# Optimization experiments

Hardware: AMD Instinct MI355X
Metric: run time of the kernel (lower is better)

Reference implementation:

```python
import jax, jax.numpy as jnp
import numpy as np

B, N, M = 8, 4096, 4096
CHAMFER_W, EMD_W, UNC_W = 1.0, 0.5, 0.01


def setup_inputs() -> dict:
    key = jax.random.key(0)
    k1, k2, k3 = jax.random.split(key, 3)
    return {
        "pred_pc": jax.random.normal(k1, (B, N, 3), dtype=jnp.float32),
        "target_pc": jax.random.normal(k2, (B, M, 3), dtype=jnp.float32),
        "uncertainty": jax.random.uniform(k3, (B, N), dtype=jnp.float32),
    }


def reference(pred_pc, target_pc, uncertainty):
    # squared pairwise distances via ||p||^2 + ||t||^2 - 2 p.t  -> [B, N, M]
    pred_sq = jnp.sum(pred_pc ** 2, axis=2, keepdims=True)            # [B, N, 1]
    tgt_sq = jnp.sum(target_pc ** 2, axis=2, keepdims=True)           # [B, M, 1]
    cross = jnp.einsum('bnd,bmd->bnm', pred_pc, target_pc)            # [B, N, M]
    d2 = pred_sq + jnp.swapaxes(tgt_sq, 1, 2) - 2.0 * cross           # [B, N, M]

    # ChamferDistanceLoss: mean of min squared dists both directions
    chamfer = jnp.mean(jnp.min(d2, axis=2)) + jnp.mean(jnp.min(d2, axis=1))

    # EMDLoss: torch.cdist p=2 (euclidean), min over targets, mean
    dist = jnp.sqrt(jnp.clip(d2, 0.0))
    emd = jnp.mean(jnp.min(dist, axis=2))

    # uncertainty regularizer
    unc_reg = jnp.mean(uncertainty) * UNC_W

    total = chamfer * CHAMFER_W + emd * EMD_W + unc_reg
    return total
```

## Files before the change

kernel.cpp:

```cpp
#include <hip/hip_runtime.h>
#include <math.h>

typedef _Float16 half8 __attribute__((ext_vector_type(8)));
typedef float    f32x4 __attribute__((ext_vector_type(4)));

#define Bb 8
#define Nn 4096
#define Mm 4096
#define BLOCK 512
#define WAVES 8
#define QB 1024
#define MB 512
#define NE 8
#define NTW 8
#define MTILES (MB / 16)
#define NQ (2 * Bb * Nn)


__global__ void __launch_bounds__(BLOCK) chamfer_mfma_kernel(
    const float* __restrict__ pred,
    const float* __restrict__ targ,
    float* __restrict__ mins)
{
    __shared__ uint4 fragA[QB];
    __shared__ uint4 fragB[MB];
    __shared__ uint4 fragZ;

    const int tid  = threadIdx.x;
    const int lane = tid & 63;
    const int wave = tid >> 6;

    const int id     = blockIdx.x;
    const int eighth = id & 7;
    const int qg     = (id >> 3) & 3;
    const int b      = (id >> 5) & 7;
    const int dir    = id >> 8;

    const float* Q = dir ? targ : pred;
    const float* T = dir ? pred : targ;

    for (int s = tid; s < QB; s += BLOCK) {
        const float* g = Q + ((size_t)b * Nn + qg * QB + s) * 3;
        _Float16 xh = (_Float16)g[0], yh = (_Float16)g[1], zh = (_Float16)g[2];
        float xq = (float)xh, yq = (float)yh, zq = (float)zh;
        float pp = fmaf(xq, xq, fmaf(yq, yq, zq * zq));
        _Float16 ph = (_Float16)pp;
        _Float16 pl = (_Float16)(pp - (float)ph);
        half8 h;
        h[0] = xh; h[1] = yh; h[2] = zh; h[3] = ph;
        h[4] = (_Float16)1.0f; h[5] = pl; h[6] = (_Float16)1.0f; h[7] = (_Float16)0.0f;
        fragA[s] = *reinterpret_cast<uint4*>(&h);
    }
    {
        const float* g = T + ((size_t)b * Mm + eighth * MB + tid) * 3;
        _Float16 xh = (_Float16)g[0], yh = (_Float16)g[1], zh = (_Float16)g[2];
        float xq = (float)xh, yq = (float)yh, zq = (float)zh;
        float tt = fmaf(xq, xq, fmaf(yq, yq, zq * zq));
        _Float16 th = (_Float16)tt;
        _Float16 tl = (_Float16)(tt - (float)th);
        const _Float16 m2 = (_Float16)(-2.0f);
        half8 h;
        h[0] = m2 * xh; h[1] = m2 * yh; h[2] = m2 * zh; h[3] = (_Float16)1.0f;
        h[4] = th; h[5] = (_Float16)1.0f; h[6] = tl; h[7] = (_Float16)0.0f;
        fragB[tid] = *reinterpret_cast<uint4*>(&h);
    }
    if (tid == 0) fragZ = make_uint4(0u, 0u, 0u, 0u);
    __syncthreads();

    const bool lo16 = (lane < 16);
    const uint4* aBase = lo16 ? &fragA[wave * NTW * 16 + lane] : &fragZ;
    const int    aStep = lo16 ? 16 : 0;
    const uint4* bBase = lo16 ? &fragB[lane] : &fragZ;
    const int    bStep = lo16 ? 16 : 0;

    half8 a[NTW];
    #pragma unroll
    for (int t = 0; t < NTW; ++t)
        a[t] = *reinterpret_cast<const half8*>(aBase + t * aStep);

    f32x4 acc[NTW];
    #pragma unroll
    for (int t = 0; t < NTW; ++t) {
        acc[t][0] = __builtin_inff(); acc[t][1] = __builtin_inff();
        acc[t][2] = __builtin_inff(); acc[t][3] = __builtin_inff();
    }

    const f32x4 cz = {0.f, 0.f, 0.f, 0.f};
    for (int j = 0; j < MTILES; j += 2) {
        half8 b0 = *reinterpret_cast<const half8*>(bBase + j * bStep);
        half8 b1 = *reinterpret_cast<const half8*>(bBase + (j + 1) * bStep);
        #pragma unroll
        for (int t = 0; t < NTW; ++t) {
            f32x4 c = __builtin_amdgcn_mfma_f32_16x16x32_f16(a[t], b0, cz, 0, 0, 0);
            f32x4 d = __builtin_amdgcn_mfma_f32_16x16x32_f16(a[t], b1, cz, 0, 0, 0);
            #pragma unroll
            for (int k = 0; k < 4; ++k)
                acc[t][k] = fminf(fminf(acc[t][k], c[k]), d[k]);
        }
    }

    #pragma unroll
    for (int t = 0; t < NTW; ++t) {
        f32x4 v = acc[t];
        #pragma unroll
        for (int m = 1; m < 16; m <<= 1) {
            #pragma unroll
            for (int k = 0; k < 4; ++k)
                v[k] = fminf(v[k], __shfl_xor(v[k], m));
        }
        if ((lane & 15) == 0) {
            const int rowbase = (lane >> 4) * 4;
            const int nloc = (wave * NTW + t) * 16 + rowbase;
            const size_t qs = ((size_t)dir * Bb + b) * Nn + qg * QB + nloc;
            #pragma unroll
            for (int k = 0; k < 4; ++k)
                mins[(qs + k) * NE + eighth] = v[k];
        }
    }
}

__global__ void __launch_bounds__(256) reduce_kernel(
    const float* __restrict__ mins, const float* __restrict__ unc,
    float* __restrict__ partials)
{
    const int q = blockIdx.x * 256 + threadIdx.x;
    const float4* m4 = (const float4*)mins;

    float4 a0 = m4[2 * q],           a1 = m4[2 * q + 1];
    float4 b0 = m4[2 * (q + 32768)], b1 = m4[2 * (q + 32768) + 1];
    float vA = fminf(fminf(fminf(a0.x, a0.y), fminf(a0.z, a0.w)),
                     fminf(fminf(a1.x, a1.y), fminf(a1.z, a1.w)));
    float vB = fminf(fminf(fminf(b0.x, b0.y), fminf(b0.z, b0.w)),
                     fminf(fminf(b1.x, b1.y), fminf(b1.z, b1.w)));
    float sA = vA, sE = sqrtf(fmaxf(vA, 0.f)), sB = vB, sU = unc[q];

    #pragma unroll
    for (int off = 32; off > 0; off >>= 1) {
        sA += __shfl_down(sA, off);  sE += __shfl_down(sE, off);
        sB += __shfl_down(sB, off);  sU += __shfl_down(sU, off);
    }
    __shared__ float sw[4][4];
    const int lane = threadIdx.x & 63, wave = threadIdx.x >> 6;
    if (lane == 0) { sw[wave][0] = sA; sw[wave][1] = sE;
                     sw[wave][2] = sB; sw[wave][3] = sU; }
    __syncthreads();
    if (threadIdx.x < 4) {
        partials[blockIdx.x * 4 + threadIdx.x] =
            sw[0][threadIdx.x] + sw[1][threadIdx.x] +
            sw[2][threadIdx.x] + sw[3][threadIdx.x];
    }
}

__global__ void __launch_bounds__(64) finalize_kernel(
    const float* __restrict__ partials, float* __restrict__ out)
{
    const float4* p4 = (const float4*)partials;
    float4 s0 = p4[threadIdx.x], s1 = p4[threadIdx.x + 64];
    float sA = s0.x + s1.x, sE = s0.y + s1.y, sB = s0.z + s1.z, sU = s0.w + s1.w;
    #pragma unroll
    for (int off = 32; off > 0; off >>= 1) {
        sA += __shfl_down(sA, off);  sE += __shfl_down(sE, off);
        sB += __shfl_down(sB, off);  sU += __shfl_down(sU, off);
    }
    if (threadIdx.x == 0) {
        const float invBN = 1.0f / (float)(Bb * Nn);
        const float invBM = 1.0f / (float)(Bb * Mm);
        out[0] = (sA * invBN + sB * invBM) + 0.5f * (sE * invBN)
               + 0.01f * (sU * invBN);
    }
}

extern "C" void kernel_launch(void* const* d_in, const int* in_sizes, int n_in,
                              void* d_out, int out_size, void* d_ws, size_t ws_size,
                              hipStream_t stream) {
    const float* pred = (const float*)d_in[0];
    const float* targ = (const float*)d_in[1];
    const float* unc  = (const float*)d_in[2];
    float* out      = (float*)d_out;
    float* mins     = (float*)d_ws;
    float* partials = (float*)d_ws + (size_t)NQ * NE;

    chamfer_mfma_kernel<<<512, BLOCK, 0, stream>>>(pred, targ, mins);
    reduce_kernel<<<128, 256, 0, stream>>>(mins, unc, partials);
    finalize_kernel<<<1, 64, 0, stream>>>(partials, out);
}
```

Measured before the change: 26.49 us.

## Fuse reduction into chamfer kernel with full-M target tiles and last-block finalize

Each block now loads all 4096 target points into LDS and processes 256 queries (2 tiles per wave), so per-query minima are complete inside a block and the intermediate mins buffer is gone. The reduce and finalize kernels are replaced by an in-kernel block sum plus an atomic counter, where the last block to finish computes the final loss. This removes two kernel launches and the global round trip for partial minima. In exchange the grid drops to 256 blocks with fewer MFMA tiles per wave, which lowers the in-flight MFMA work available to hide latency. The counter also relies on the workspace starting at zero, and it wraps modulo the grid size instead of being reset.

```diff
diff --git a/kernel.cpp b/kernel.cpp
--- a/kernel.cpp
+++ b/kernel.cpp
@@ -9,50 +9,42 @@
 #define Mm 4096
 #define BLOCK 512
 #define WAVES 8
-#define QB 1024
-#define MB 512
-#define NE 8
-#define NTW 8
-#define MTILES (MB / 16)
-#define NQ (2 * Bb * Nn)
+#define QB 256
+#define NTW 2
+#define MTILES (Mm / 16)
+#define GRID 256
 
-
-__global__ void __launch_bounds__(BLOCK) chamfer_mfma_kernel(
+__global__ void __launch_bounds__(BLOCK) chamfer_fused_kernel(
     const float* __restrict__ pred,
     const float* __restrict__ targ,
-    float* __restrict__ mins)
+    const float* __restrict__ unc,
+    float4* __restrict__ psum,
+    unsigned* __restrict__ counter,
+    float* __restrict__ out)
 {
-    __shared__ uint4 fragA[QB];
-    __shared__ uint4 fragB[MB];
-    __shared__ uint4 fragZ;
+    __shared__ uint4 fragB[Mm];
+    float* wsum = (float*)fragB;
 
     const int tid  = threadIdx.x;
     const int lane = tid & 63;
     const int wave = tid >> 6;
 
-    const int id     = blockIdx.x;
-    const int eighth = id & 7;
-    const int qg     = (id >> 3) & 3;
-    const int b      = (id >> 5) & 7;
-    const int dir    = id >> 8;
+    const int id  = blockIdx.x;
+    const int qt  = id & 15;
+    const int b   = (id >> 4) & 7;
+    const int dir = id >> 7;
 
     const float* Q = dir ? targ : pred;
     const float* T = dir ? pred : targ;
 
-    for (int s = tid; s < QB; s += BLOCK) {
-        const float* g = Q + ((size_t)b * Nn + qg * QB + s) * 3;
-        _Float16 xh = (_Float16)g[0], yh = (_Float16)g[1], zh = (_Float16)g[2];
-        float xq = (float)xh, yq = (float)yh, zq = (float)zh;
-        float pp = fmaf(xq, xq, fmaf(yq, yq, zq * zq));
-        _Float16 ph = (_Float16)pp;
-        _Float16 pl = (_Float16)(pp - (float)ph);
-        half8 h;
-        h[0] = xh; h[1] = yh; h[2] = zh; h[3] = ph;
-        h[4] = (_Float16)1.0f; h[5] = pl; h[6] = (_Float16)1.0f; h[7] = (_Float16)0.0f;
-        fragA[s] = *reinterpret_cast<uint4*>(&h);
+    float su = 0.f;
+    if (tid < 32) {
+        float4 uu = ((const float4*)unc)[id * 32 + tid];
+        su = (uu.x + uu.y) + (uu.z + uu.w);
     }
-    {
-        const float* g = T + ((size_t)b * Mm + eighth * MB + tid) * 3;
+
+    for (int s = tid; s < Mm; s += BLOCK) {
+        const float* g = T + ((size_t)b * Mm + s) * 3;
         _Float16 xh = (_Float16)g[0], yh = (_Float16)g[1], zh = (_Float16)g[2];
         float xq = (float)xh, yq = (float)yh, zq = (float)zh;
         float tt = fmaf(xq, xq, fmaf(yq, yq, zq * zq));
@@ -62,111 +54,127 @@
         half8 h;
         h[0] = m2 * xh; h[1] = m2 * yh; h[2] = m2 * zh; h[3] = (_Float16)1.0f;
         h[4] = th; h[5] = (_Float16)1.0f; h[6] = tl; h[7] = (_Float16)0.0f;
-        fragB[tid] = *reinterpret_cast<uint4*>(&h);
+        fragB[s] = *reinterpret_cast<uint4*>(&h);
     }
-    if (tid == 0) fragZ = make_uint4(0u, 0u, 0u, 0u);
+
+    const bool lo16 = (lane < 16);
+    half8 a[NTW];
+    #pragma unroll
+    for (int t = 0; t < NTW; ++t) {
+        half8 h;
+        #pragma unroll
+        for (int e = 0; e < 8; ++e) h[e] = (_Float16)0.0f;
+        if (lo16) {
+            const int n = qt * QB + (wave * NTW + t) * 16 + lane;
+            const float* g = Q + ((size_t)b * Nn + n) * 3;
+            _Float16 xh = (_Float16)g[0], yh = (_Float16)g[1], zh = (_Float16)g[2];
+            float xq = (float)xh, yq = (float)yh, zq = (float)zh;
+            float pp = fmaf(xq, xq, fmaf(yq, yq, zq * zq));
+            _Float16 ph = (_Float16)pp;
+            _Float16 pl = (_Float16)(pp - (float)ph);
+            h[0] = xh; h[1] = yh; h[2] = zh; h[3] = ph;
+            h[4] = (_Float16)1.0f; h[5] = pl; h[6] = (_Float16)1.0f; h[7] = (_Float16)0.0f;
+        }
+        a[t] = h;
+    }
     __syncthreads();
 
-    const bool lo16 = (lane < 16);
-    const uint4* aBase = lo16 ? &fragA[wave * NTW * 16 + lane] : &fragZ;
-    const int    aStep = lo16 ? 16 : 0;
-    const uint4* bBase = lo16 ? &fragB[lane] : &fragZ;
-    const int    bStep = lo16 ? 16 : 0;
-
-    half8 a[NTW];
-    #pragma unroll
-    for (int t = 0; t < NTW; ++t)
-        a[t] = *reinterpret_cast<const half8*>(aBase + t * aStep);
-
-    f32x4 acc[NTW];
-    #pragma unroll
-    for (int t = 0; t < NTW; ++t) {
-        acc[t][0] = __builtin_inff(); acc[t][1] = __builtin_inff();
-        acc[t][2] = __builtin_inff(); acc[t][3] = __builtin_inff();
-    }
-
+    const int col = lane & 15;
     const f32x4 cz = {0.f, 0.f, 0.f, 0.f};
+    const float inf = __builtin_inff();
+    f32x4 acc0 = {inf, inf, inf, inf}, acc1 = acc0;
+    #pragma unroll 4
     for (int j = 0; j < MTILES; j += 2) {
-        half8 b0 = *reinterpret_cast<const half8*>(bBase + j * bStep);
-        half8 b1 = *reinterpret_cast<const half8*>(bBase + (j + 1) * bStep);
+        half8 b0 = *reinterpret_cast<const half8*>(&fragB[(j << 4) + col]);
+        half8 b1 = *reinterpret_cast<const half8*>(&fragB[((j + 1) << 4) + col]);
+        f32x4 c00 = __builtin_amdgcn_mfma_f32_16x16x32_f16(a[0], b0, cz, 0, 0, 0);
+        f32x4 c01 = __builtin_amdgcn_mfma_f32_16x16x32_f16(a[0], b1, cz, 0, 0, 0);
+        f32x4 c10 = __builtin_amdgcn_mfma_f32_16x16x32_f16(a[1], b0, cz, 0, 0, 0);
+        f32x4 c11 = __builtin_amdgcn_mfma_f32_16x16x32_f16(a[1], b1, cz, 0, 0, 0);
         #pragma unroll
-        for (int t = 0; t < NTW; ++t) {
-            f32x4 c = __builtin_amdgcn_mfma_f32_16x16x32_f16(a[t], b0, cz, 0, 0, 0);
-            f32x4 d = __builtin_amdgcn_mfma_f32_16x16x32_f16(a[t], b1, cz, 0, 0, 0);
-            #pragma unroll
-            for (int k = 0; k < 4; ++k)
-                acc[t][k] = fminf(fminf(acc[t][k], c[k]), d[k]);
+        for (int k = 0; k < 4; ++k) {
+            acc0[k] = fminf(fminf(acc0[k], c00[k]), c01[k]);
+            acc1[k] = fminf(fminf(acc1[k], c10[k]), c11[k]);
         }
     }
 
+    float s1 = 0.f, s2 = 0.f;
     #pragma unroll
     for (int t = 0; t < NTW; ++t) {
-        f32x4 v = acc[t];
+        f32x4 v = t ? acc1 : acc0;
         #pragma unroll
         for (int m = 1; m < 16; m <<= 1) {
             #pragma unroll
             for (int k = 0; k < 4; ++k)
                 v[k] = fminf(v[k], __shfl_xor(v[k], m));
         }
-        if ((lane & 15) == 0) {
-            const int rowbase = (lane >> 4) * 4;
-            const int nloc = (wave * NTW + t) * 16 + rowbase;
-            const size_t qs = ((size_t)dir * Bb + b) * Nn + qg * QB + nloc;
+        if (col == 0) {
             #pragma unroll
-            for (int k = 0; k < 4; ++k)
-                mins[(qs + k) * NE + eighth] = v[k];
+            for (int k = 0; k < 4; ++k) {
+                const float d2 = v[k];
+                s1 += d2;
+                s2 += sqrtf(fmaxf(d2, 0.f));
+            }
         }
     }
-}
+    #pragma unroll
+    for (int m = 1; m < 64; m <<= 1) {
+        s1 += __shfl_xor(s1, m);
+        s2 += __shfl_xor(s2, m);
+        su += __shfl_xor(su, m);
+    }
 
-__global__ void __launch_bounds__(256) reduce_kernel(
-    const float* __restrict__ mins, const float* __restrict__ unc,
-    float* __restrict__ partials)
-{
-    const int q = blockIdx.x * 256 + threadIdx.x;
-    const float4* m4 = (const float4*)mins;
-
-    float4 a0 = m4[2 * q],           a1 = m4[2 * q + 1];
-    float4 b0 = m4[2 * (q + 32768)], b1 = m4[2 * (q + 32768) + 1];
-    float vA = fminf(fminf(fminf(a0.x, a0.y), fminf(a0.z, a0.w)),
-                     fminf(fminf(a1.x, a1.y), fminf(a1.z, a1.w)));
-    float vB = fminf(fminf(fminf(b0.x, b0.y), fminf(b0.z, b0.w)),
-                     fminf(fminf(b1.x, b1.y), fminf(b1.z, b1.w)));
-    float sA = vA, sE = sqrtf(fmaxf(vA, 0.f)), sB = vB, sU = unc[q];
-
-    #pragma unroll
-    for (int off = 32; off > 0; off >>= 1) {
-        sA += __shfl_down(sA, off);  sE += __shfl_down(sE, off);
-        sB += __shfl_down(sB, off);  sU += __shfl_down(sU, off);
+    __syncthreads();
+    if (lane == 0) {
+        wsum[wave * 4 + 0] = s1;
+        wsum[wave * 4 + 1] = s2;
+        wsum[wave * 4 + 2] = su;
     }
-    __shared__ float sw[4][4];
-    const int lane = threadIdx.x & 63, wave = threadIdx.x >> 6;
-    if (lane == 0) { sw[wave][0] = sA; sw[wave][1] = sE;
-                     sw[wave][2] = sB; sw[wave][3] = sU; }
     __syncthreads();
-    if (threadIdx.x < 4) {
-        partials[blockIdx.x * 4 + threadIdx.x] =
-            sw[0][threadIdx.x] + sw[1][threadIdx.x] +
-            sw[2][threadIdx.x] + sw[3][threadIdx.x];
+    if (tid == 0) {
+        float S1 = 0.f, S2 = 0.f, SU = 0.f;
+        #pragma unroll
+        for (int w = 0; w < WAVES; ++w) {
+            S1 += wsum[w * 4 + 0]; S2 += wsum[w * 4 + 1]; SU += wsum[w * 4 + 2];
+        }
+        psum[id] = make_float4(S1, S2, SU, 0.f);
+        __threadfence();
+        unsigned old = atomicAdd(counter, 1u);
+        ((int*)wsum)[32] = (((old + 1) & (GRID - 1)) == 0) ? 1 : 0;
     }
-}
-
-__global__ void __launch_bounds__(64) finalize_kernel(
-    const float* __restrict__ partials, float* __restrict__ out)
-{
-    const float4* p4 = (const float4*)partials;
-    float4 s0 = p4[threadIdx.x], s1 = p4[threadIdx.x + 64];
-    float sA = s0.x + s1.x, sE = s0.y + s1.y, sB = s0.z + s1.z, sU = s0.w + s1.w;
-    #pragma unroll
-    for (int off = 32; off > 0; off >>= 1) {
-        sA += __shfl_down(sA, off);  sE += __shfl_down(sE, off);
-        sB += __shfl_down(sB, off);  sU += __shfl_down(sU, off);
-    }
-    if (threadIdx.x == 0) {
-        const float invBN = 1.0f / (float)(Bb * Nn);
-        const float invBM = 1.0f / (float)(Bb * Mm);
-        out[0] = (sA * invBN + sB * invBM) + 0.5f * (sE * invBN)
-               + 0.01f * (sU * invBN);
+    __syncthreads();
+    if (((int*)wsum)[32]) {
+        __threadfence();
+        float sa = 0.f, sb = 0.f, se = 0.f, sU = 0.f;
+        if (tid < GRID) {
+            float4 v = psum[tid];
+            if (tid < GRID / 2) { sa = v.x; se = v.y; }
+            else                { sb = v.x; }
+            sU = v.z;
+        }
+        #pragma unroll
+        for (int m = 1; m < 64; m <<= 1) {
+            sa += __shfl_xor(sa, m); sb += __shfl_xor(sb, m);
+            se += __shfl_xor(se, m); sU += __shfl_xor(sU, m);
+        }
+        __syncthreads();
+        if (lane == 0) {
+            wsum[wave * 4 + 0] = sa; wsum[wave * 4 + 1] = sb;
+            wsum[wave * 4 + 2] = se; wsum[wave * 4 + 3] = sU;
+        }
+        __syncthreads();
+        if (tid == 0) {
+            float SA = 0.f, SB = 0.f, SE = 0.f, SU2 = 0.f;
+            #pragma unroll
+            for (int w = 0; w < WAVES; ++w) {
+                SA += wsum[w * 4 + 0]; SB += wsum[w * 4 + 1];
+                SE += wsum[w * 4 + 2]; SU2 += wsum[w * 4 + 3];
+            }
+            const float invBN = 1.0f / (float)(Bb * Nn);
+            const float invBM = 1.0f / (float)(Bb * Mm);
+            out[0] = (SA * invBN + SB * invBM) + 0.5f * (SE * invBN)
+                   + 0.01f * (SU2 * invBN);
+        }
     }
 }
 
@@ -176,11 +184,11 @@
     const float* pred = (const float*)d_in[0];
     const float* targ = (const float*)d_in[1];
     const float* unc  = (const float*)d_in[2];
-    float* out      = (float*)d_out;
-    float* mins     = (float*)d_ws;
-    float* partials = (float*)d_ws + (size_t)NQ * NE;
+    float* out = (float*)d_out;
 
-    chamfer_mfma_kernel<<<512, BLOCK, 0, stream>>>(pred, targ, mins);
-    reduce_kernel<<<128, 256, 0, stream>>>(mins, unc, partials);
-    finalize_kernel<<<1, 64, 0, stream>>>(partials, out);
+    float4*   psum    = (float4*)d_ws;
+    unsigned* counter = (unsigned*)((char*)d_ws + 4096);
+
+    chamfer_fused_kernel<<<GRID, BLOCK, 0, stream>>>(pred, targ, unc,
+                                                     psum, counter, out);
 }
```

After: 26.35 us. Within noise of the previous version (-0.5%).

## Switch distance tiles to 32x32x16 MFMA with DPP row-min reduction

Applied to the files above, without the earlier changes.

Replaces the 16x16x32 MFMA tiling, in which only 16 lanes carried real data and the rest read a zero fragment, with 32x32x16 MFMA where 32 lanes hold query and target fragments. It also changes the grid to 1024 blocks of 256 threads, each covering 256 queries against 1024 targets. Query fragments are built directly in registers and the cross-lane min uses DPP instead of shuffles. The partial-min buffer shrinks from 8 to 4 slices per query, so the reduce kernel reads half as much. This is meant to waste fewer MFMA lanes per useful product and raise occupancy, at the cost of re-reading target tiles more often.

```diff
diff --git a/kernel.cpp b/kernel.cpp
--- a/kernel.cpp
+++ b/kernel.cpp
@@ -1,59 +1,61 @@
 #include <hip/hip_runtime.h>
 #include <math.h>
 
-typedef _Float16 half8 __attribute__((ext_vector_type(8)));
-typedef float    f32x4 __attribute__((ext_vector_type(4)));
+typedef _Float16 half8  __attribute__((ext_vector_type(8)));
+typedef float    f32x16 __attribute__((ext_vector_type(16)));
 
 #define Bb 8
 #define Nn 4096
 #define Mm 4096
-#define BLOCK 512
-#define WAVES 8
-#define QB 1024
-#define MB 512
-#define NE 8
-#define NTW 8
-#define MTILES (MB / 16)
+#define BLOCK 256
+#define WAVES 4
+#define NTA 2
+#define QBLK 256
+#define TBLK 1024
+#define MT (TBLK / 32)
+#define MS 4
+#define QTILES (Nn / QBLK)
 #define NQ (2 * Bb * Nn)
 
+template<int CTRL>
+__device__ __forceinline__ float dppmin(float v) {
+    int iv = __float_as_int(v);
+    iv = __builtin_amdgcn_update_dpp(iv, iv, CTRL, 0xF, 0xF, false);
+    return fminf(v, __int_as_float(iv));
+}
+__device__ __forceinline__ float rowmin32(float v) {
+    v = dppmin<0xB1>(v);
+    v = dppmin<0x4E>(v);
+    v = dppmin<0x141>(v);
+    v = dppmin<0x140>(v);
+    v = fminf(v, __shfl_xor(v, 16));
+    return v;
+}
 
-__global__ void __launch_bounds__(BLOCK) chamfer_mfma_kernel(
+
+__global__ void __launch_bounds__(BLOCK) chamfer_mfma32_kernel(
     const float* __restrict__ pred,
     const float* __restrict__ targ,
     float* __restrict__ mins)
 {
-    __shared__ uint4 fragA[QB];
-    __shared__ uint4 fragB[MB];
-    __shared__ uint4 fragZ;
+    __shared__ uint4 fragB[TBLK];
 
     const int tid  = threadIdx.x;
     const int lane = tid & 63;
     const int wave = tid >> 6;
 
-    const int id     = blockIdx.x;
-    const int eighth = id & 7;
-    const int qg     = (id >> 3) & 3;
-    const int b      = (id >> 5) & 7;
-    const int dir    = id >> 8;
+    const int id  = blockIdx.x;
+    const int ms  = id & 3;
+    const int qt  = (id >> 2) & 15;
+    const int b   = (id >> 6) & 7;
+    const int dir = id >> 9;
 
     const float* Q = dir ? targ : pred;
     const float* T = dir ? pred : targ;
 
-    for (int s = tid; s < QB; s += BLOCK) {
-        const float* g = Q + ((size_t)b * Nn + qg * QB + s) * 3;
-        _Float16 xh = (_Float16)g[0], yh = (_Float16)g[1], zh = (_Float16)g[2];
-        float xq = (float)xh, yq = (float)yh, zq = (float)zh;
-        float pp = fmaf(xq, xq, fmaf(yq, yq, zq * zq));
-        _Float16 ph = (_Float16)pp;
-        _Float16 pl = (_Float16)(pp - (float)ph);
-        half8 h;
-        h[0] = xh; h[1] = yh; h[2] = zh; h[3] = ph;
-        h[4] = (_Float16)1.0f; h[5] = pl; h[6] = (_Float16)1.0f; h[7] = (_Float16)0.0f;
-        fragA[s] = *reinterpret_cast<uint4*>(&h);
-    }
-    {
-        const float* g = T + ((size_t)b * Mm + eighth * MB + tid) * 3;
-        _Float16 xh = (_Float16)g[0], yh = (_Float16)g[1], zh = (_Float16)g[2];
+    for (int s = tid; s < TBLK; s += BLOCK) {
+        const float* gp = T + ((size_t)b * Mm + ms * TBLK + s) * 3;
+        _Float16 xh = (_Float16)gp[0], yh = (_Float16)gp[1], zh = (_Float16)gp[2];
         float xq = (float)xh, yq = (float)yh, zq = (float)zh;
         float tt = fmaf(xq, xq, fmaf(yq, yq, zq * zq));
         _Float16 th = (_Float16)tt;
@@ -62,59 +64,64 @@
         half8 h;
         h[0] = m2 * xh; h[1] = m2 * yh; h[2] = m2 * zh; h[3] = (_Float16)1.0f;
         h[4] = th; h[5] = (_Float16)1.0f; h[6] = tl; h[7] = (_Float16)0.0f;
-        fragB[tid] = *reinterpret_cast<uint4*>(&h);
+        fragB[s] = *reinterpret_cast<uint4*>(&h);
     }
-    if (tid == 0) fragZ = make_uint4(0u, 0u, 0u, 0u);
+
+    const int qbase = qt * QBLK + wave * (NTA * 32);
+    half8 a0, a1;
+    #pragma unroll
+    for (int e = 0; e < 8; ++e) { a0[e] = (_Float16)0.0f; a1[e] = (_Float16)0.0f; }
+    if (lane < 32) {
+        #pragma unroll
+        for (int t = 0; t < NTA; ++t) {
+            const int n = qbase + t * 32 + lane;
+            const float* gp = Q + ((size_t)b * Nn + n) * 3;
+            _Float16 xh = (_Float16)gp[0], yh = (_Float16)gp[1], zh = (_Float16)gp[2];
+            float xq = (float)xh, yq = (float)yh, zq = (float)zh;
+            float pp = fmaf(xq, xq, fmaf(yq, yq, zq * zq));
+            _Float16 ph = (_Float16)pp;
+            _Float16 pl = (_Float16)(pp - (float)ph);
+            half8 h;
+            h[0] = xh; h[1] = yh; h[2] = zh; h[3] = ph;
+            h[4] = (_Float16)1.0f; h[5] = pl; h[6] = (_Float16)1.0f; h[7] = (_Float16)0.0f;
+            if (t == 0) a0 = h; else a1 = h;
+        }
+    }
     __syncthreads();
 
-    const bool lo16 = (lane < 16);
-    const uint4* aBase = lo16 ? &fragA[wave * NTW * 16 + lane] : &fragZ;
-    const int    aStep = lo16 ? 16 : 0;
-    const uint4* bBase = lo16 ? &fragB[lane] : &fragZ;
-    const int    bStep = lo16 ? 16 : 0;
+    const int col = lane & 31;
+    const f32x16 cz = {};
+    const float inf = __builtin_inff();
+    f32x16 acc0, acc1;
+    #pragma unroll
+    for (int k = 0; k < 16; ++k) { acc0[k] = inf; acc1[k] = inf; }
 
-    half8 a[NTW];
-    #pragma unroll
-    for (int t = 0; t < NTW; ++t)
-        a[t] = *reinterpret_cast<const half8*>(aBase + t * aStep);
-
-    f32x4 acc[NTW];
-    #pragma unroll
-    for (int t = 0; t < NTW; ++t) {
-        acc[t][0] = __builtin_inff(); acc[t][1] = __builtin_inff();
-        acc[t][2] = __builtin_inff(); acc[t][3] = __builtin_inff();
+    for (int j = 0; j < MT; j += 2) {
+        half8 b0 = *reinterpret_cast<const half8*>(&fragB[(j << 5) + col]);
+        half8 b1 = *reinterpret_cast<const half8*>(&fragB[((j + 1) << 5) + col]);
+        f32x16 c0 = __builtin_amdgcn_mfma_f32_32x32x16_f16(a0, b0, cz, 0, 0, 0);
+        f32x16 c1 = __builtin_amdgcn_mfma_f32_32x32x16_f16(a0, b1, cz, 0, 0, 0);
+        #pragma unroll
+        for (int k = 0; k < 16; ++k)
+            acc0[k] = fminf(fminf(acc0[k], c0[k]), c1[k]);
+        f32x16 d0 = __builtin_amdgcn_mfma_f32_32x32x16_f16(a1, b0, cz, 0, 0, 0);
+        f32x16 d1 = __builtin_amdgcn_mfma_f32_32x32x16_f16(a1, b1, cz, 0, 0, 0);
+        #pragma unroll
+        for (int k = 0; k < 16; ++k)
+            acc1[k] = fminf(fminf(acc1[k], d0[k]), d1[k]);
     }
 
-    const f32x4 cz = {0.f, 0.f, 0.f, 0.f};
-    for (int j = 0; j < MTILES; j += 2) {
-        half8 b0 = *reinterpret_cast<const half8*>(bBase + j * bStep);
-        half8 b1 = *reinterpret_cast<const half8*>(bBase + (j + 1) * bStep);
-        #pragma unroll
-        for (int t = 0; t < NTW; ++t) {
-            f32x4 c = __builtin_amdgcn_mfma_f32_16x16x32_f16(a[t], b0, cz, 0, 0, 0);
-            f32x4 d = __builtin_amdgcn_mfma_f32_16x16x32_f16(a[t], b1, cz, 0, 0, 0);
-            #pragma unroll
-            for (int k = 0; k < 4; ++k)
-                acc[t][k] = fminf(fminf(acc[t][k], c[k]), d[k]);
-        }
-    }
-
+    const int hi = lane >> 5;
+    const size_t qoff = ((size_t)dir * Bb + b) * Nn;
     #pragma unroll
-    for (int t = 0; t < NTW; ++t) {
-        f32x4 v = acc[t];
-        #pragma unroll
-        for (int m = 1; m < 16; m <<= 1) {
-            #pragma unroll
-            for (int k = 0; k < 4; ++k)
-                v[k] = fminf(v[k], __shfl_xor(v[k], m));
-        }
-        if ((lane & 15) == 0) {
-            const int rowbase = (lane >> 4) * 4;
-            const int nloc = (wave * NTW + t) * 16 + rowbase;
-            const size_t qs = ((size_t)dir * Bb + b) * Nn + qg * QB + nloc;
-            #pragma unroll
-            for (int k = 0; k < 4; ++k)
-                mins[(qs + k) * NE + eighth] = v[k];
+    for (int r = 0; r < 16; ++r) {
+        float v0 = rowmin32(acc0[r]);
+        float v1 = rowmin32(acc1[r]);
+        if (col == 0) {
+            const int rl = (r & 3) + 8 * (r >> 2) + 4 * hi;
+            const size_t q0 = qoff + qbase + rl;
+            mins[q0 * MS + ms]        = v0;
+            mins[(q0 + 32) * MS + ms] = v1;
         }
     }
 }
@@ -126,12 +133,10 @@
     const int q = blockIdx.x * 256 + threadIdx.x;
     const float4* m4 = (const float4*)mins;
 
-    float4 a0 = m4[2 * q],           a1 = m4[2 * q + 1];
-    float4 b0 = m4[2 * (q + 32768)], b1 = m4[2 * (q + 32768) + 1];
-    float vA = fminf(fminf(fminf(a0.x, a0.y), fminf(a0.z, a0.w)),
-                     fminf(fminf(a1.x, a1.y), fminf(a1.z, a1.w)));
-    float vB = fminf(fminf(fminf(b0.x, b0.y), fminf(b0.z, b0.w)),
-                     fminf(fminf(b1.x, b1.y), fminf(b1.z, b1.w)));
+    float4 a4 = m4[q];
+    float4 b4 = m4[q + 32768];
+    float vA = fminf(fminf(a4.x, a4.y), fminf(a4.z, a4.w));
+    float vB = fminf(fminf(b4.x, b4.y), fminf(b4.z, b4.w));
     float sA = vA, sE = sqrtf(fmaxf(vA, 0.f)), sB = vB, sU = unc[q];
 
     #pragma unroll
@@ -178,9 +183,9 @@
     const float* unc  = (const float*)d_in[2];
     float* out      = (float*)d_out;
     float* mins     = (float*)d_ws;
-    float* partials = (float*)d_ws + (size_t)NQ * NE;
+    float* partials = (float*)d_ws + (size_t)NQ * MS;
 
-    chamfer_mfma_kernel<<<512, BLOCK, 0, stream>>>(pred, targ, mins);
+    chamfer_mfma32_kernel<<<1024, BLOCK, 0, stream>>>(pred, targ, mins);
     reduce_kernel<<<128, 256, 0, stream>>>(mins, unc, partials);
     finalize_kernel<<<1, 64, 0, stream>>>(partials, out);
 }
```

After: 25.93 us. 2.1% less time.
